# Optimization experiments

Measured on AMD Instinct MI355X. Metric: run time of the kernel, lower is better.

The kernel has to match this reference:

```python
import jax, jax.numpy as jnp
import numpy as np

NUM_ITERS = 3
EPS = 1e-8


def squash(t, axis=-1):
    sq = jnp.sum(t * t, axis=axis, keepdims=True)
    scale = sq / (1.0 + sq)
    return scale * t / jnp.sqrt(sq + EPS)


def setup_inputs() -> dict:
    key = jax.random.key(0)
    k1, k2 = jax.random.split(key)
    B, Nin, Din, Nout, Dout = 32, 2048, 16, 64, 32
    x = jax.random.normal(k1, (B, Nin, Din), dtype=jnp.float32)
    W = jax.random.normal(k2, (1, Nin, Nout, Dout, Din), dtype=jnp.float32)
    return {"x": x, "W": W}


def reference(x, W):
    # x: [B, Nin, Din]; W: [1, Nin, Nout, Dout, Din]
    # u_hat[b,n,o,d] = sum_i W[0,n,o,d,i] * x[b,n,i]
    u_hat = jnp.einsum('nodi,bni->bnod', W[0], x)  # [B, Nin, Nout, Dout]
    B, Nin, Nout, _ = u_hat.shape
    b = jnp.zeros((B, Nin, Nout, 1), dtype=u_hat.dtype)
    v = None
    for it in range(NUM_ITERS):
        c = jax.nn.softmax(b, axis=2)              # [B, Nin, Nout, 1]
        s = jnp.sum(c * u_hat, axis=1)             # [B, Nout, Dout]
        v = squash(s, axis=-1)                     # [B, Nout, Dout]
        if it < NUM_ITERS - 1:
            agreement = jnp.sum(u_hat * v[:, None], axis=-1, keepdims=True)
            b = b + agreement
    return v
```

## Files before the change

kernel.cpp:

```cpp
#include <hip/hip_runtime.h>


#define B_   32
#define NIN  2048
#define DIN  16
#define NOUT 64
#define DOUT 32
#define BQ   8
#define NCHB 16
#define CG   (NIN / NCHB)
#define NBLK (CG * (B_ / BQ))
#define TPB  1024
#define PART_PER_BLK (BQ * NOUT * DOUT / 2)
#define NC2   16
#define NCHK2 (NIN / NC2)
#define NBLK2 ((B_ / 8) * NCHK2)
#define TPB2  512

__device__ __forceinline__ unsigned pack_bf16(float a, float b) {
    unsigned ia = __float_as_uint(a), ib = __float_as_uint(b);
    ia += 0x7fffu + ((ia >> 16) & 1u);
    ib += 0x7fffu + ((ib >> 16) & 1u);
    return (ia >> 16) | (ib & 0xffff0000u);
}

__global__ __launch_bounds__(TPB)
void caps_pass1u(const float* __restrict__ W, const float* __restrict__ x,
                 unsigned* __restrict__ uws, float2* __restrict__ part)
{
    const int t  = threadIdx.x;
    const int o  = t & 63;
    const int dg = t >> 6;
    const int d0 = dg << 1;

    const int bid  = blockIdx.x;
    const int xcd  = bid & 7;
    const int j    = bid >> 3;
    const int cg   = xcd * (CG / 8) + (j >> 2);
    const int quad = j & 3;
    const int nbase = cg * NCHB;
    const int bbase = quad * BQ;

    __shared__ float4 xs[BQ][NCHB * DIN / 4];

    if (t < BQ * NCHB * DIN / 4) {
        const int bb = t >> 6;
        const int k  = t & 63;
        xs[bb][k] = ((const float4*)x)[(size_t)(bbase + bb) * (NIN * DIN / 4)
                                       + (size_t)nbase * (DIN / 4) + k];
    }

    float acc0[BQ], acc1[BQ];
#pragma unroll
    for (int bb = 0; bb < BQ; ++bb) { acc0[bb] = 0.f; acc1[bb] = 0.f; }

    __syncthreads();

    for (int nn = 0; nn < NCHB; ++nn) {
        const int n = nbase + nn;
        const float4* wp = (const float4*)(W +
            (((size_t)n * NOUT + o) * DOUT + d0) * DIN);
        float4 w[8];
#pragma unroll
        for (int q = 0; q < 8; ++q) w[q] = wp[q];
        unsigned* urow = uws + (((size_t)bbase * NIN + n) * 16 + dg) * 64 + o;
#pragma unroll
        for (int bb = 0; bb < BQ; ++bb) {
            const float4* xr = &xs[bb][nn * 4];
            float u0 = 0.f, u1 = 0.f;
#pragma unroll
            for (int q = 0; q < 4; ++q) {
                const float4 xv = xr[q];
                u0 += w[q].x*xv.x + w[q].y*xv.y + w[q].z*xv.z + w[q].w*xv.w;
                u1 += w[4+q].x*xv.x + w[4+q].y*xv.y + w[4+q].z*xv.z + w[4+q].w*xv.w;
            }
            acc0[bb] += u0;
            acc1[bb] += u1;
            urow[(size_t)bb * (NIN * 1024)] = pack_bf16(u0, u1);
        }
    }

#pragma unroll
    for (int bb = 0; bb < BQ; ++bb) {
        float2* base = part + (size_t)(cg * 4 + quad) * PART_PER_BLK;
        base[bb * (NOUT * DOUT / 2) + o * (DOUT / 2) + dg] =
            make_float2(acc0[bb] * (1.0f / 64.0f), acc1[bb] * (1.0f / 64.0f));
    }
}

__global__ __launch_bounds__(TPB2)
void caps_pass23u(const unsigned* __restrict__ uws, const float* __restrict__ v_in,
                  float* __restrict__ part2)
{
    const int t    = threadIdx.x;
    const int o    = t & 63;
    const int wid  = t >> 6;

    const int bid   = blockIdx.x;
    const int b     = (bid >> 7) * 8 + wid;
    const int chunk = bid & 127;
    const int nbase = chunk * NC2;

    float vr[DOUT];
    {
        const float4* vp = (const float4*)(v_in + ((size_t)b * NOUT + o) * DOUT);
#pragma unroll
        for (int q = 0; q < 8; ++q) {
            const float4 vv = vp[q];
            vr[q*4+0] = vv.x; vr[q*4+1] = vv.y; vr[q*4+2] = vv.z; vr[q*4+3] = vv.w;
        }
    }

    float acc[DOUT];
#pragma unroll
    for (int d = 0; d < DOUT; ++d) acc[d] = 0.f;

    const unsigned* ub = uws + (((size_t)b * NIN + nbase) * 16) * 64 + o;

#pragma unroll 1
    for (int nn = 0; nn < NC2; ++nn) {
        const unsigned* un = ub + (size_t)nn * 1024;
        unsigned up[16];
#pragma unroll
        for (int dg = 0; dg < 16; ++dg) up[dg] = un[dg * 64];

        float logit = 0.f;
#pragma unroll
        for (int dg = 0; dg < 16; ++dg) {
            const float uE = __uint_as_float(up[dg] << 16);
            const float uO = __uint_as_float(up[dg] & 0xffff0000u);
            logit += uE * vr[2*dg] + uO * vr[2*dg+1];
        }
        const float e = __expf(logit);
        float sm = e;
#pragma unroll
        for (int m = 1; m < 64; m <<= 1) sm += __shfl_xor(sm, m);
        const float c = e / sm;
#pragma unroll
        for (int dg = 0; dg < 16; ++dg) {
            const float uE = __uint_as_float(up[dg] << 16);
            const float uO = __uint_as_float(up[dg] & 0xffff0000u);
            acc[2*dg]   += c * uE;
            acc[2*dg+1] += c * uO;
        }
    }

    float* pb = part2 + (((size_t)b * NCHK2 + chunk) * NOUT + o) * DOUT;
#pragma unroll
    for (int d = 0; d < DOUT; d += 4)
        *(float4*)(pb + d) = make_float4(acc[d], acc[d+1], acc[d+2], acc[d+3]);
}

__global__ __launch_bounds__(256)
void reduce_squash2(const float* __restrict__ part2, float* __restrict__ vout,
                    int accumulate)
{
    const int id = blockIdx.x * 256 + threadIdx.x;
    const float* p = part2 + (size_t)(id >> 11) * (NCHK2 * NOUT * DOUT) + (id & 2047);
    float s = 0.f;
#pragma unroll 8
    for (int ch = 0; ch < NCHK2; ++ch) s += p[(size_t)ch * (NOUT * DOUT)];

    float sq = s * s;
#pragma unroll
    for (int m = 1; m < 32; m <<= 1) sq += __shfl_xor(sq, m);
    const float f = sq / ((1.0f + sq) * sqrtf(sq + 1e-8f));
    const float v = s * f;
    if (accumulate) vout[id] += v;
    else            vout[id] = v;
}

template<int PASS, bool ATOMIC>
__global__ __launch_bounds__(TPB)
void caps_pass(const float* __restrict__ W, const float* __restrict__ x,
               const float* __restrict__ v_in, float* __restrict__ s_out,
               float2* __restrict__ part)
{
    const int t    = threadIdx.x;
    const int o    = t >> 4;
    const int dg   = t & 15;
    const int d0   = dg << 1;
    const int lane = t & 63;
    const int wid  = t >> 6;

    const int bid  = blockIdx.x;
    const int xcd  = bid & 7;
    const int j    = bid >> 3;
    const int cg   = xcd * (CG / 8) + (j >> 2);
    const int quad = j & 3;
    const int nbase = cg * NCHB;
    const int bbase = quad * BQ;

    __shared__ float4 xs[BQ][NCHB * DIN / 4];

    if (t < BQ * NCHB * DIN / 4) {
        const int bb = t >> 6;
        const int k  = t & 63;
        xs[bb][k] = ((const float4*)x)[(size_t)(bbase + bb) * (NIN * DIN / 4)
                                       + (size_t)nbase * (DIN / 4) + k];
    }

    float acc0[BQ], acc1[BQ];
#pragma unroll
    for (int bb = 0; bb < BQ; ++bb) { acc0[bb] = 0.f; acc1[bb] = 0.f; }

    __syncthreads();

    if constexpr (PASS == 1) {
        for (int nn = 0; nn < NCHB; ++nn) {
            const float4* wp = (const float4*)(W +
                (((size_t)(nbase + nn) * NOUT + o) * DOUT + d0) * DIN);
            float4 w[8];
#pragma unroll
            for (int q = 0; q < 8; ++q) w[q] = wp[q];
#pragma unroll
            for (int bb = 0; bb < BQ; ++bb) {
                const float4* xr = &xs[bb][nn * 4];
                float u0 = 0.f, u1 = 0.f;
#pragma unroll
                for (int q = 0; q < 4; ++q) {
                    const float4 xv = xr[q];
                    u0 += w[q].x*xv.x + w[q].y*xv.y + w[q].z*xv.z + w[q].w*xv.w;
                    u1 += w[4+q].x*xv.x + w[4+q].y*xv.y + w[4+q].z*xv.z + w[4+q].w*xv.w;
                }
                acc0[bb] += u0;
                acc1[bb] += u1;
            }
        }
    } else {
        __shared__ float  lg[BQ * NOUT];
        __shared__ float  cs[BQ * NOUT];
        __shared__ float2 ustash[BQ][TPB];
        for (int nn = 0; nn < NCHB; ++nn) {
            const float4* wp = (const float4*)(W +
                (((size_t)(nbase + nn) * NOUT + o) * DOUT + d0) * DIN);
            float4 w[8];
#pragma unroll
            for (int q = 0; q < 8; ++q) w[q] = wp[q];
#pragma unroll
            for (int bb = 0; bb < BQ; ++bb) {
                const float4* xr = &xs[bb][nn * 4];
                float u0 = 0.f, u1 = 0.f;
#pragma unroll
                for (int q = 0; q < 4; ++q) {
                    const float4 xv = xr[q];
                    u0 += w[q].x*xv.x + w[q].y*xv.y + w[q].z*xv.z + w[q].w*xv.w;
                    u1 += w[4+q].x*xv.x + w[4+q].y*xv.y + w[4+q].z*xv.z + w[4+q].w*xv.w;
                }
                const float2 vvv = ((const float2*)v_in)[
                    (size_t)(bbase + bb) * (NOUT * DOUT / 2) + o * (DOUT / 2) + dg];
                float p = u0 * vvv.x + u1 * vvv.y;
                p += __shfl_xor(p, 1);
                p += __shfl_xor(p, 2);
                p += __shfl_xor(p, 4);
                p += __shfl_xor(p, 8);
                if (dg == 0) lg[bb * NOUT + o] = p;
                ustash[bb][t] = make_float2(u0, u1);
            }
            __syncthreads();
            if (wid < BQ) {
                const float e = __expf(lg[wid * NOUT + lane]);
                float sm = e;
#pragma unroll
                for (int m = 1; m < 64; m <<= 1) sm += __shfl_xor(sm, m);
                cs[wid * NOUT + lane] = e / sm;
            }
            __syncthreads();
#pragma unroll
            for (int bb = 0; bb < BQ; ++bb) {
                const float c = cs[bb * NOUT + o];
                const float2 u = ustash[bb][t];
                acc0[bb] += c * u.x;
                acc1[bb] += c * u.y;
            }
        }
    }

    const float scale = (PASS == 1) ? (1.0f / 64.0f) : 1.0f;
    if constexpr (ATOMIC) {
#pragma unroll
        for (int bb = 0; bb < BQ; ++bb) {
            float* dst = &s_out[((size_t)(bbase + bb) * NOUT + o) * DOUT + d0];
            atomicAdd(dst,     acc0[bb] * scale);
            atomicAdd(dst + 1, acc1[bb] * scale);
        }
    } else {
        float2* base = part + (size_t)(cg * 4 + quad) * PART_PER_BLK;
#pragma unroll
        for (int bb = 0; bb < BQ; ++bb)
            base[bb * (NOUT * DOUT / 2) + o * (DOUT / 2) + dg] =
                make_float2(acc0[bb] * scale, acc1[bb] * scale);
    }
}

__global__ __launch_bounds__(256)
void reduce_squash(const float2* __restrict__ part, float* __restrict__ vout,
                   int accumulate)
{
    const int id = blockIdx.x * 256 + threadIdx.x;
    const int dg = id & 15;
    const int o  = (id >> 4) & 63;
    const int b  = id >> 10;
    const int quad = b >> 3, bb = b & 7;
    const size_t base = (size_t)bb * (NOUT * DOUT / 2) + o * (DOUT / 2) + dg;

    float2 a0 = make_float2(0.f, 0.f), a1 = make_float2(0.f, 0.f);
    for (int cg = 0; cg < CG; cg += 2) {
        const float2 p0 = part[(size_t)(cg * 4 + quad) * PART_PER_BLK + base];
        const float2 p1 = part[(size_t)((cg + 1) * 4 + quad) * PART_PER_BLK + base];
        a0.x += p0.x; a0.y += p0.y;
        a1.x += p1.x; a1.y += p1.y;
    }
    const float sx = a0.x + a1.x, sy = a0.y + a1.y;

    float sq = sx * sx + sy * sy;
    sq += __shfl_xor(sq, 1);
    sq += __shfl_xor(sq, 2);
    sq += __shfl_xor(sq, 4);
    sq += __shfl_xor(sq, 8);
    const float f = sq / ((1.0f + sq) * sqrtf(sq + 1e-8f));

    float2* vo = (float2*)vout;
    float2 r = make_float2(sx * f, sy * f);
    if (accumulate) {
        const float2 old = vo[id];
        r.x += old.x; r.y += old.y;
    }
    vo[id] = r;
}

__global__ void squash_k(const float* __restrict__ s, float* __restrict__ vout,
                         int accumulate)
{
    const int idx = blockIdx.x * 256 + threadIdx.x;
    const float val = s[idx];
    float sq = val * val;
#pragma unroll
    for (int m = 1; m < 32; m <<= 1) sq += __shfl_xor(sq, m);
    const float f = sq / ((1.0f + sq) * sqrtf(sq + 1e-8f));
    const float v = val * f;
    if (accumulate) vout[idx] += v;
    else            vout[idx] = v;
}

extern "C" void kernel_launch(void* const* d_in, const int* in_sizes, int n_in,
                              void* d_out, int out_size, void* d_ws, size_t ws_size,
                              hipStream_t stream)
{
    (void)in_sizes; (void)n_in; (void)out_size;
    const float* x = (const float*)d_in[0];
    const float* W = (const float*)d_in[1];
    float* out = (float*)d_out;

    const size_t uBytes    = (size_t)B_ * NIN * NOUT * DOUT * 2;
    const size_t partBytes = (size_t)NBLK * PART_PER_BLK * sizeof(float2);
    const size_t vBytes    = (size_t)B_ * NOUT * DOUT * sizeof(float);

    if (ws_size >= uBytes + partBytes + vBytes) {
        unsigned* uws  = (unsigned*)d_ws;
        float2*   p1   = (float2*)((char*)d_ws + uBytes);
        float*    p2   = (float*)p1;
        float*    vA   = (float*)((char*)d_ws + uBytes + partBytes);

        caps_pass1u<<<dim3(NBLK), dim3(TPB), 0, stream>>>(W, x, uws, p1);
        reduce_squash<<<dim3(128), dim3(256), 0, stream>>>(p1, vA, 0);

        caps_pass23u<<<dim3(NBLK2), dim3(TPB2), 0, stream>>>(uws, vA, p2);
        reduce_squash2<<<dim3(256), dim3(256), 0, stream>>>(p2, vA, 1);

        caps_pass23u<<<dim3(NBLK2), dim3(TPB2), 0, stream>>>(uws, vA, p2);
        reduce_squash2<<<dim3(256), dim3(256), 0, stream>>>(p2, out, 0);
    } else if (ws_size >= partBytes + vBytes) {
        float2* part = (float2*)d_ws;
        float*  vA   = (float*)((char*)d_ws + partBytes);

        caps_pass<1, false><<<dim3(NBLK), dim3(TPB), 0, stream>>>(W, x, nullptr, nullptr, part);
        reduce_squash<<<dim3(128), dim3(256), 0, stream>>>(part, vA, 0);

        caps_pass<2, false><<<dim3(NBLK), dim3(TPB), 0, stream>>>(W, x, vA, nullptr, part);
        reduce_squash<<<dim3(128), dim3(256), 0, stream>>>(part, vA, 1);

        caps_pass<2, false><<<dim3(NBLK), dim3(TPB), 0, stream>>>(W, x, vA, nullptr, part);
        reduce_squash<<<dim3(128), dim3(256), 0, stream>>>(part, out, 0);
    } else {
        float* s  = (float*)d_ws;
        float* vA = s + B_ * NOUT * DOUT;

        hipMemsetAsync(s, 0, vBytes, stream);
        caps_pass<1, true><<<dim3(NBLK), dim3(TPB), 0, stream>>>(W, x, nullptr, s, nullptr);
        squash_k<<<dim3(256), dim3(256), 0, stream>>>(s, vA, 0);

        hipMemsetAsync(s, 0, vBytes, stream);
        caps_pass<2, true><<<dim3(NBLK), dim3(TPB), 0, stream>>>(W, x, vA, s, nullptr);
        squash_k<<<dim3(256), dim3(256), 0, stream>>>(s, vA, 1);

        hipMemsetAsync(s, 0, vBytes, stream);
        caps_pass<2, true><<<dim3(NBLK), dim3(TPB), 0, stream>>>(W, x, vA, s, nullptr);
        squash_k<<<dim3(256), dim3(256), 0, stream>>>(s, out, 0);
    }
}
```

Baseline: 374.9 us.

## Transpose bf16 u_hat workspace to output-major layout for vectorized loads

Changes the packed u_hat workspace from [b][n][dg][o] to [b][n][o][dg]. The first pass now maps threads with o as the outer index, so each thread writes its packed pair at a contiguous offset and W rows are read more contiguously across neighbouring threads. The routing pass can then fetch a thread's 16 packed values with four 128-bit loads instead of sixteen strided 32-bit loads. This is meant to cut load-instruction count and improve access efficiency. Any other kernel that still reads the workspace with the old indexing would break.

Result: faster. 347.6 us (-7.3%).

```diff
diff --git a/kernel.cpp b/kernel.cpp
--- a/kernel.cpp
+++ b/kernel.cpp
@@ -29,8 +29,8 @@
                  unsigned* __restrict__ uws, float2* __restrict__ part)
 {
     const int t  = threadIdx.x;
-    const int o  = t & 63;
-    const int dg = t >> 6;
+    const int o  = t >> 4;
+    const int dg = t & 15;
     const int d0 = dg << 1;
 
     const int bid  = blockIdx.x;
@@ -63,7 +63,6 @@
         float4 w[8];
 #pragma unroll
         for (int q = 0; q < 8; ++q) w[q] = wp[q];
-        unsigned* urow = uws + (((size_t)bbase * NIN + n) * 16 + dg) * 64 + o;
 #pragma unroll
         for (int bb = 0; bb < BQ; ++bb) {
             const float4* xr = &xs[bb][nn * 4];
@@ -76,7 +75,7 @@
             }
             acc0[bb] += u0;
             acc1[bb] += u1;
-            urow[(size_t)bb * (NIN * 1024)] = pack_bf16(u0, u1);
+            uws[((size_t)(bbase + bb) * NIN + n) * 1024 + t] = pack_bf16(u0, u1);
         }
     }
 
@@ -115,21 +114,21 @@
 #pragma unroll
     for (int d = 0; d < DOUT; ++d) acc[d] = 0.f;
 
-    const unsigned* ub = uws + (((size_t)b * NIN + nbase) * 16) * 64 + o;
+    const uint4* ub = (const uint4*)(uws + ((size_t)b * NIN + nbase) * 1024) + o * 4;
 
 #pragma unroll 1
     for (int nn = 0; nn < NC2; ++nn) {
-        const unsigned* un = ub + (size_t)nn * 1024;
-        unsigned up[16];
-#pragma unroll
-        for (int dg = 0; dg < 16; ++dg) up[dg] = un[dg * 64];
+        const uint4* un = ub + (size_t)nn * 256;
+        const uint4 p0 = un[0], p1 = un[1], p2 = un[2], p3 = un[3];
+        unsigned up[16] = { p0.x, p0.y, p0.z, p0.w,  p1.x, p1.y, p1.z, p1.w,
+                            p2.x, p2.y, p2.z, p2.w,  p3.x, p3.y, p3.z, p3.w };
 
         float logit = 0.f;
 #pragma unroll
-        for (int dg = 0; dg < 16; ++dg) {
-            const float uE = __uint_as_float(up[dg] << 16);
-            const float uO = __uint_as_float(up[dg] & 0xffff0000u);
-            logit += uE * vr[2*dg] + uO * vr[2*dg+1];
+        for (int k = 0; k < 16; ++k) {
+            const float uE = __uint_as_float(up[k] << 16);
+            const float uO = __uint_as_float(up[k] & 0xffff0000u);
+            logit += uE * vr[2*k] + uO * vr[2*k+1];
         }
         const float e = __expf(logit);
         float sm = e;
@@ -137,11 +136,11 @@
         for (int m = 1; m < 64; m <<= 1) sm += __shfl_xor(sm, m);
         const float c = e / sm;
 #pragma unroll
-        for (int dg = 0; dg < 16; ++dg) {
-            const float uE = __uint_as_float(up[dg] << 16);
-            const float uO = __uint_as_float(up[dg] & 0xffff0000u);
-            acc[2*dg]   += c * uE;
-            acc[2*dg+1] += c * uO;
+        for (int k = 0; k < 16; ++k) {
+            const float uE = __uint_as_float(up[k] << 16);
+            const float uO = __uint_as_float(up[k] & 0xffff0000u);
+            acc[2*k]   += c * uE;
+            acc[2*k+1] += c * uO;
         }
     }
 
```
